# Kernel optimization log

Measured on AMD Instinct MI355X. Metric: run time of the kernel, lower is better.

Reference implementation:

```python
import jax, jax.numpy as jnp
import numpy as np

B, S, D, H, K, R = 16, 512, 768, 12, 16, 32
NS = 128  # LSH sample size = min(128, S//2)
HD = D // H

def _ln(t, g, b):
    m = t.mean(-1, keepdims=True)
    v = t.var(-1, keepdims=True)
    return (t - m) / jnp.sqrt(v + 1e-5) * g + b

def setup_inputs() -> dict:
    key = jax.random.key(0)
    ks = jax.random.split(key, 16)
    n = lambda k, shp: jax.random.normal(k, shp, jnp.float32) * 0.02
    return {
        'x': jax.random.normal(ks[0], (B, S, D), jnp.float32),
        'sample_idx': jax.random.randint(ks[1], (NS,), 0, S, jnp.int32),
        'w1': n(ks[2], (6, D // 4)), 'b1': jnp.zeros(D // 4, jnp.float32),
        'w2': n(ks[3], (D // 4, R)), 'b2': jnp.zeros(R, jnp.float32),
        'wd0': n(ks[4], (R, R)), 'bd0': jnp.zeros(R, jnp.float32),
        'wd1': n(ks[5], (R, R)), 'bd1': jnp.zeros(R, jnp.float32),
        'in_proj_w': n(ks[6], (D, 3 * D)), 'in_proj_b': jnp.zeros(3 * D, jnp.float32),
        'out_proj_w': n(ks[7], (D, D)), 'out_proj_b': jnp.zeros(D, jnp.float32),
        'topo_w': n(ks[8], (R, D)), 'topo_b': jnp.zeros(D, jnp.float32),
        'topo_gate': jnp.float32(0.1),
        'ln1_g': jnp.ones(D, jnp.float32), 'ln1_b': jnp.zeros(D, jnp.float32),
        'ln2_g': jnp.ones(D, jnp.float32), 'ln2_b': jnp.zeros(D, jnp.float32),
        'ffn_w1': n(ks[9], (D, 2 * D)), 'ffn_b1': jnp.zeros(2 * D, jnp.float32),
        'ffn_w2': n(ks[10], (2 * D, D)), 'ffn_b2': jnp.zeros(D, jnp.float32),
    }

def reference(x, sample_idx, w1, b1, w2, b2, wd0, bd0, wd1, bd1,
              in_proj_w, in_proj_b, out_proj_w, out_proj_b,
              topo_w, topo_b, topo_gate, ln1_g, ln1_b, ln2_g, ln2_b,
              ffn_w1, ffn_b1, ffn_w2, ffn_b2):
    # --- FastLSH._lsh_knn (S > 256 path): cdist to 128 sampled tokens + topk smallest ---
    s = jnp.take(x, sample_idx, axis=1)                                   # [B,NS,D]
    d2 = (jnp.sum(x * x, -1)[:, :, None] + jnp.sum(s * s, -1)[:, None, :]
          - 2.0 * jnp.einsum('bnd,bmd->bnm', x, s))                       # [B,S,NS]
    dist = jnp.sqrt(jnp.maximum(d2, 0.0))
    neg_top, _nbr = jax.lax.top_k(-dist, K)
    knn_dist = -neg_top                                                   # [B,S,K]
    # --- SimplifiedPersistenceComputer: scalar stats per batch (torch uses .item(), detached) ---
    df = knn_dist.reshape(B, -1)
    mean = df.mean(1); std = df.std(1, ddof=1)                            # torch.std is unbiased
    mn = df.min(1); mx = df.max(1)
    stats0 = jax.lax.stop_gradient(
        jnp.stack([mean, std, mn, mx, mean / 2, std / 2], -1))            # [B,6]
    # --- FastPersistenceLandscape: only dim-0 landscape feeds attention ---
    land0 = (jax.nn.relu(stats0 @ w1 + b1) @ w2 + b2) @ wd0 + bd0         # [B,R]
    # --- TopologicalAttention: MHA self-attention + gated topo embedding ---
    qkv = x @ in_proj_w + in_proj_b                                       # [B,S,3D]
    q, k, v = jnp.split(qkv, 3, axis=-1)
    hsplit = lambda t: t.reshape(B, S, H, HD).transpose(0, 2, 1, 3)
    q, k, v = hsplit(q), hsplit(k), hsplit(v)
    p = jax.nn.softmax(jnp.einsum('bhqd,bhkd->bhqk', q, k) / jnp.sqrt(jnp.float32(HD)), -1)
    o = jnp.einsum('bhqk,bhkd->bhqd', p, v).transpose(0, 2, 1, 3).reshape(B, S, D)
    attn = o @ out_proj_w + out_proj_b
    topo = land0 @ topo_w + topo_b                                        # [B,D]
    attn_out = attn + topo_gate * topo[:, None, :]
    # --- post-norm residual + FFN (GELU exact) ---
    x1 = _ln(x + attn_out, ln1_g, ln1_b)
    ffn = jax.nn.gelu(x1 @ ffn_w1 + ffn_b1, approximate=False) @ ffn_w2 + ffn_b2
    return _ln(x1 + ffn, ln2_g, ln2_b)
```

## Files before the change

### kernel.cpp

```cpp
#include <hip/hip_runtime.h>
#include <math.h>

#define Bz 16
#define Sz 512
#define Dz 768
#define Hz 12
#define HDz 64
#define Kz 16
#define NSz 128
#define Rz 32

typedef __attribute__((ext_vector_type(4))) float f32x4;
typedef __attribute__((ext_vector_type(8))) short bf16x8;

__device__ __forceinline__ unsigned short f2bf(float f) {
    unsigned u = __float_as_uint(f);
    return (unsigned short)((u + 0x7fffu + ((u >> 16) & 1u)) >> 16);
}
__device__ __forceinline__ float bf2f(unsigned short s) {
    return __uint_as_float(((unsigned)s) << 16);
}
__device__ __forceinline__ unsigned pk2(float a, float b) {
    return (unsigned)f2bf(a) | ((unsigned)f2bf(b) << 16);
}
__device__ __forceinline__ void gload_lds16(const void* g, void* l) {
    __builtin_amdgcn_global_load_lds(
        (const __attribute__((address_space(1))) unsigned int*)g,
        (__attribute__((address_space(3))) unsigned int*)l, 16, 0, 0);
}

__global__ __launch_bounds__(256) void xrn_k(const float* __restrict__ x, short* __restrict__ xb,
                                             float* __restrict__ xsq) {
    int wv = threadIdx.x >> 6, lane = threadIdx.x & 63;
    int row = blockIdx.x * 4 + wv;
    const float* r = x + (size_t)row * Dz;
    unsigned long long* dst = (unsigned long long*)(xb + (size_t)row * Dz);
    float s = 0.f;
#pragma unroll
    for (int j = 0; j < 3; j++) {
        float4 v = ((const float4*)r)[lane + j * 64];
        s += v.x * v.x + v.y * v.y + v.z * v.z + v.w * v.w;
        dst[lane + j * 64] = (unsigned long long)pk2(v.x, v.y) | ((unsigned long long)pk2(v.z, v.w) << 32);
    }
#pragma unroll
    for (int off = 32; off > 0; off >>= 1) s += __shfl_xor(s, off, 64);
    if (lane == 0) xsq[row] = s;
}

__device__ __forceinline__ void wtrans_body(const float* __restrict__ src, short* __restrict__ dst,
                                            int K, int N, int k0, int n0, int tid,
                                            float (*t)[65]) {
#pragma unroll
    for (int i = 0; i < 16; i++) {
        int e = tid + 256 * i;
        int kk = e >> 6, nn = e & 63;
        t[kk][nn] = src[(size_t)(k0 + kk) * N + n0 + nn];
    }
    __syncthreads();
#pragma unroll
    for (int i = 0; i < 16; i++) {
        int e = tid + 256 * i;
        int nn = e >> 6, kk = e & 63;
        dst[(size_t)(n0 + nn) * K + k0 + kk] = (short)f2bf(t[kk][nn]);
    }
}

__global__ __launch_bounds__(256) void prep_k(const float* __restrict__ ipw, const float* __restrict__ opw,
                                              const float* __restrict__ f1w, const float* __restrict__ f2w,
                                              short* __restrict__ wT_ip, short* __restrict__ wT_op,
                                              short* __restrict__ wT_f1, short* __restrict__ wT_f2,
                                              const float* __restrict__ x, const int* __restrict__ sidx,
                                              short* __restrict__ scb) {
    __shared__ float t[64][65];
    int bid = blockIdx.x, tid = threadIdx.x;
    if (bid < 432) {
        int lo = bid, tx = lo % 36, ty = lo / 36;
        wtrans_body(ipw, wT_ip, Dz, 3 * Dz, ty * 64, tx * 64, tid, t);
    } else if (bid < 576) {
        int lo = bid - 432, tx = lo % 12, ty = lo / 12;
        wtrans_body(opw, wT_op, Dz, Dz, ty * 64, tx * 64, tid, t);
    } else if (bid < 864) {
        int lo = bid - 576, tx = lo % 24, ty = lo / 24;
        wtrans_body(f1w, wT_f1, Dz, 2 * Dz, ty * 64, tx * 64, tid, t);
    } else if (bid < 1152) {
        int lo = bid - 864, tx = lo % 12, ty = lo / 12;
        wtrans_body(f2w, wT_f2, 2 * Dz, Dz, ty * 64, tx * 64, tid, t);
    } else {
        int gb = bid - 1152;
        int row = gb * 16 + (tid >> 4);
        int b = row >> 7, jj = row & 127;
        const float* src = x + ((size_t)(b * Sz) + sidx[jj]) * Dz;
        unsigned long long* dr = (unsigned long long*)(scb + (size_t)row * Dz);
        int l16 = tid & 15;
#pragma unroll
        for (int j = 0; j < 12; j++) {
            int idx = j * 16 + l16;
            float4 v = ((const float4*)src)[idx];
            dr[idx] = (unsigned long long)pk2(v.x, v.y) | ((unsigned long long)pk2(v.z, v.w) << 32);
        }
    }
}

__global__ __launch_bounds__(128) void knnstat_k(const float* __restrict__ D, float4* __restrict__ rowred) {
    __shared__ float dv[NSz];
    __shared__ float red[NSz], red2[NSz];
    __shared__ float rmin, rmax;
    int tid = threadIdx.x, row = blockIdx.x;
    float dist = D[(size_t)row * NSz + tid];
    dv[tid] = dist;
    __syncthreads();
    int rank = 0;
#pragma unroll 8
    for (int j = 0; j < NSz; j++) {
        float o = dv[j];
        rank += (o < dist) || (o == dist && j < tid);
    }
    if (rank == 0) rmin = dist;
    if (rank == Kz - 1) rmax = dist;
    red[tid] = (rank < Kz) ? dist : 0.f;
    red2[tid] = (rank < Kz) ? dist * dist : 0.f;
    __syncthreads();
    for (int st = 64; st > 0; st >>= 1) {
        if (tid < st) { red[tid] += red[tid + st]; red2[tid] += red2[tid + st]; }
        __syncthreads();
    }
    if (tid == 0) rowred[row] = make_float4(red[0], red2[0], rmin, rmax);
}

__global__ __launch_bounds__(256) void land_topo_k(const float4* __restrict__ rowred,
                                                   const float* __restrict__ w1, const float* __restrict__ b1,
                                                   const float* __restrict__ w2, const float* __restrict__ b2,
                                                   const float* __restrict__ wd0, const float* __restrict__ bd0,
                                                   const float* __restrict__ topo_w, const float* __restrict__ topo_b,
                                                   const float* gate, float* __restrict__ topo_add) {
    __shared__ float4 red4[256];
    __shared__ float st[6];
    __shared__ float h[Dz / 4];
    __shared__ float l2[Rz];
    __shared__ float land[Rz];
    int b = blockIdx.x, tid = threadIdx.x;
    float4 a = rowred[b * Sz + tid];
    float4 c = rowred[b * Sz + 256 + tid];
    float4 r;
    r.x = a.x + c.x; r.y = a.y + c.y;
    r.z = fminf(a.z, c.z); r.w = fmaxf(a.w, c.w);
    red4[tid] = r;
    __syncthreads();
    for (int stp = 128; stp > 0; stp >>= 1) {
        if (tid < stp) {
            float4 p = red4[tid], q = red4[tid + stp];
            p.x += q.x; p.y += q.y; p.z = fminf(p.z, q.z); p.w = fmaxf(p.w, q.w);
            red4[tid] = p;
        }
        __syncthreads();
    }
    if (tid == 0) {
        const double N = (double)(Sz * Kz);
        double sum = (double)red4[0].x, sumsq = (double)red4[0].y;
        double mean = sum / N;
        double var = (sumsq - N * mean * mean) / (N - 1.0);
        float sd = (float)sqrt(fmax(var, 0.0));
        float m = (float)mean;
        st[0] = m; st[1] = sd;
        st[2] = red4[0].z; st[3] = red4[0].w;
        st[4] = m * 0.5f; st[5] = sd * 0.5f;
    }
    __syncthreads();
    if (tid < Dz / 4) {
        float a1 = b1[tid];
#pragma unroll
        for (int i = 0; i < 6; i++) a1 += st[i] * w1[i * (Dz / 4) + tid];
        h[tid] = fmaxf(a1, 0.f);
    }
    __syncthreads();
    if (tid < Rz) {
        float a1 = b2[tid];
        for (int i = 0; i < Dz / 4; i++) a1 += h[i] * w2[i * Rz + tid];
        l2[tid] = a1;
    }
    __syncthreads();
    if (tid < Rz) {
        float a1 = bd0[tid];
#pragma unroll
        for (int i = 0; i < Rz; i++) a1 += l2[i] * wd0[i * Rz + tid];
        land[tid] = a1;
    }
    __syncthreads();
    float g = gate[0];
    for (int d = tid; d < Dz; d += 256) {
        float a1 = topo_b[d];
#pragma unroll
        for (int i = 0; i < Rz; i++) a1 += land[i] * topo_w[i * Dz + d];
        topo_add[b * Dz + d] = g * a1;
    }
}

__device__ __forceinline__ void stage_tile(const short* gbase, int ldk, int row0, int k0,
                                           short* ldsbase, int w, int l) {
#pragma unroll
    for (int c = 0; c < 2; c++) {
        int r = c * 64 + w * 16 + (l >> 2);
        int qg = (l & 3) ^ ((r >> 1) & 3);
        const short* src = gbase + (size_t)(row0 + r) * ldk + k0 + qg * 8;
        gload_lds16(src, ldsbase + (c * 4 + w) * 512);
    }
}

template <int EPI>
__global__ __launch_bounds__(256) void mgemm_k(const short* __restrict__ A, const short* __restrict__ BT,
                                               const float* __restrict__ bias,
                                               float* __restrict__ C, short* __restrict__ Cb,
                                               int N, int Kd, int gx,
                                               short* __restrict__ qo, short* __restrict__ ko,
                                               short* __restrict__ vT,
                                               const int* __restrict__ sidx, const float* __restrict__ xsq) {
    __shared__ short lds[2][2][4096];
    int tid = threadIdx.x, w = tid >> 6, l = tid & 63;
    int nwg = gridDim.x, q = nwg >> 3;
    int orig = (blockIdx.x & 7) * q + (blockIdx.x >> 3);
    int m0 = (orig / gx) * 128, n0 = (orig % gx) * 128;
    const short* BTb = BT;
    if (EPI == 4) BTb += (size_t)(m0 >> 9) * NSz * Kd;
    int wr = w >> 1, wc = w & 1, g = l >> 4, ql = l & 15;
    f32x4 acc[4][4];
#pragma unroll
    for (int i = 0; i < 4; i++)
#pragma unroll
        for (int j = 0; j < 4; j++) acc[i][j] = (f32x4){0.f, 0.f, 0.f, 0.f};
    stage_tile(A, Kd, m0, 0, lds[0][0], w, l);
    stage_tile(BTb, Kd, n0, 0, lds[0][1], w, l);
    __syncthreads();
    int nst = Kd / 32;
    for (int t = 0; t < nst; t++) {
        int buf = t & 1;
        if (t + 1 < nst) {
            stage_tile(A, Kd, m0, (t + 1) * 32, lds[buf ^ 1][0], w, l);
            stage_tile(BTb, Kd, n0, (t + 1) * 32, lds[buf ^ 1][1], w, l);
        }
        bf16x8 af[4], bfr[4];
#pragma unroll
        for (int i = 0; i < 4; i++) {
            int r = wr * 64 + i * 16 + ql;
            af[i] = *(const bf16x8*)((const char*)lds[buf][0] + r * 64 + ((g ^ ((r >> 1) & 3)) << 4));
        }
#pragma unroll
        for (int j = 0; j < 4; j++) {
            int r = wc * 64 + j * 16 + ql;
            bfr[j] = *(const bf16x8*)((const char*)lds[buf][1] + r * 64 + ((g ^ ((r >> 1) & 3)) << 4));
        }
#pragma unroll
        for (int i = 0; i < 4; i++)
#pragma unroll
            for (int j = 0; j < 4; j++)
                acc[i][j] = __builtin_amdgcn_mfma_f32_16x16x32_bf16(af[i], bfr[j], acc[i][j], 0, 0, 0);
        __syncthreads();
    }

    if (EPI == 4) {
#pragma unroll
        for (int i = 0; i < 4; i++) {
            int rowb = m0 + wr * 64 + i * 16 + g * 4;
#pragma unroll
            for (int j = 0; j < 4; j++) {
                int col = wc * 64 + j * 16 + ql;
                float ssq = xsq[((rowb >> 9) << 9) + sidx[col]];
#pragma unroll
                for (int r = 0; r < 4; r++) {
                    int row = rowb + r;
                    float d2 = xsq[row] + ssq - 2.f * acc[i][j][r];
                    C[(size_t)row * NSz + col] = sqrtf(fmaxf(d2, 0.f));
                }
            }
        }
    } else {
        short* cl = (short*)lds;
        const int part = (EPI == 2) ? (n0 / Dz) : 0;
        const bool cm = (EPI == 2) && (part == 2);
        if (!cm) {
#pragma unroll
            for (int i = 0; i < 4; i++) {
#pragma unroll
                for (int j = 0; j < 4; j++) {
                    int colL = wc * 64 + j * 16 + ql;
                    float bsv = bias[n0 + colL];
#pragma unroll
                    for (int r = 0; r < 4; r++) {
                        int rowL = wr * 64 + i * 16 + g * 4 + r;
                        float val = acc[i][j][r] + bsv;
                        if (EPI == 1) val = 0.5f * val * (1.f + erff(val * 0.70710678118654752f));
                        cl[rowL * 128 + (((colL >> 3) ^ (rowL & 15)) << 3) + (colL & 7)] = (short)f2bf(val);
                    }
                }
            }
        } else {
#pragma unroll
            for (int i = 0; i < 4; i++) {
#pragma unroll
                for (int j = 0; j < 4; j++) {
                    int colL = wc * 64 + j * 16 + ql;
                    float bsv = bias[n0 + colL];
                    int row4 = wr * 64 + i * 16 + g * 4;
                    unsigned long long u =
                        (unsigned long long)pk2(acc[i][j][0] + bsv, acc[i][j][1] + bsv)
                      | ((unsigned long long)pk2(acc[i][j][2] + bsv, acc[i][j][3] + bsv) << 32);
                    *(unsigned long long*)((char*)cl +
                        colL * 256 + (((row4 >> 3) ^ (colL & 15)) << 4) + (row4 & 7) * 2) = u;
                }
            }
        }
        __syncthreads();
#pragma unroll
        for (int it = 0; it < 8; it++) {
            int c = tid + 256 * it;
            int a = c >> 4, sl = c & 15;
            bf16x8 vv = *(const bf16x8*)(cl + a * 128 + ((sl ^ (a & 15)) << 3));
            if (EPI == 1 || EPI == 3) {
                *(bf16x8*)(Cb + (size_t)(m0 + a) * N + n0 + sl * 8) = vv;
            } else if (!cm) {
                int rr = m0 + a;
                int b = rr >> 9, s = rr & 511;
                int h = ((n0 % Dz) >> 6) + (sl >> 3);
                short* dst = part ? ko : qo;
                *(bf16x8*)(dst + (((size_t)(b * Hz + h)) * Sz + s) * HDz + (sl & 7) * 8) = vv;
            } else {
                int wi = (n0 - 2 * Dz) + a;
                int h = wi >> 6, hd = wi & 63;
                int b = m0 >> 9, s0 = (m0 & 511) + sl * 8;
                *(bf16x8*)(vT + ((size_t)(b * Hz + h) * HDz + hd) * Sz + s0) = vv;
            }
        }
    }
}

__global__ __launch_bounds__(256, 4) void attn4_k(const short* __restrict__ Q, const short* __restrict__ Kt,
                                                  const short* __restrict__ Vt, short* __restrict__ O) {
    __shared__ short kl[2][4096];
    __shared__ short vl[2][4096];
    __shared__ char plds[4][2048];
    int tid = threadIdx.x, w = tid >> 6, l = tid & 63;
    int bh = blockIdx.x % (Bz * Hz), qt = blockIdx.x / (Bz * Hz);
    int g = l >> 4, ql = l & 15;
    const short* qb = Q + (size_t)bh * (Sz * HDz) + (size_t)(qt * 64 + w * 16) * HDz;
    const short* kb = Kt + (size_t)bh * (Sz * HDz);
    const short* vb = Vt + (size_t)bh * (HDz * Sz);
    bf16x8 qf0 = *(const bf16x8*)(qb + (size_t)ql * HDz + g * 8);
    bf16x8 qf1 = *(const bf16x8*)(qb + (size_t)ql * HDz + 32 + g * 8);
    f32x4 oa[4];
#pragma unroll
    for (int m = 0; m < 4; m++) oa[m] = (f32x4){0.f, 0.f, 0.f, 0.f};
    float psum = 0.f;

    auto stage = [&](int c, int bb) {
#pragma unroll
        for (int it = 0; it < 2; it++) {
            int i = (it * 4 + w) * 64 + l;
            int row = i >> 3;
            int ss = (i & 7) ^ (row & 7);
            gload_lds16(kb + (size_t)(c * 64 + row) * HDz + ss * 8,
                        (char*)kl[bb] + (it * 4 + w) * 1024);
            gload_lds16(vb + (size_t)row * Sz + c * 64 + ss * 8,
                        (char*)vl[bb] + (it * 4 + w) * 1024);
        }
    };

    stage(0, 0);
    __syncthreads();
    char* pw = plds[w];
#pragma unroll
    for (int c = 0; c < 8; c++) {
        int cur = c & 1;
        if (c < 7) stage(c + 1, cur ^ 1);
        const char* kc = (const char*)kl[cur];
        const char* vc = (const char*)vl[cur];
#pragma unroll
        for (int tl = 0; tl < 4; tl++) {
            int row = tl * 16 + ql;
            bf16x8 a0 = *(const bf16x8*)(kc + row * 128 + ((g ^ (ql & 7)) << 4));
            bf16x8 a1 = *(const bf16x8*)(kc + row * 128 + (((4 + g) ^ (ql & 7)) << 4));
            f32x4 s4 = (f32x4){0.f, 0.f, 0.f, 0.f};
            s4 = __builtin_amdgcn_mfma_f32_16x16x32_bf16(a0, qf0, s4, 0, 0, 0);
            s4 = __builtin_amdgcn_mfma_f32_16x16x32_bf16(a1, qf1, s4, 0, 0, 0);
            float e0 = __expf(s4[0] * 0.125f);
            float e1 = __expf(s4[1] * 0.125f);
            float e2 = __expf(s4[2] * 0.125f);
            float e3 = __expf(s4[3] * 0.125f);
            psum += (e0 + e1) + (e2 + e3);
            int slot = (tl * 2 + (g >> 1)) ^ (ql & 7);
            *(unsigned long long*)(pw + ql * 128 + slot * 16 + (g & 1) * 8)
                = (unsigned long long)pk2(e0, e1) | ((unsigned long long)pk2(e2, e3) << 32);
        }
#pragma unroll
        for (int s = 0; s < 2; s++) {
            int slot = (s * 4 + g) ^ (ql & 7);
            bf16x8 pb = *(const bf16x8*)(pw + ql * 128 + slot * 16);
#pragma unroll
            for (int m = 0; m < 4; m++) {
                int row = m * 16 + ql;
                bf16x8 va = *(const bf16x8*)(vc + row * 128 + (((s * 4 + g) ^ (ql & 7)) << 4));
                oa[m] = __builtin_amdgcn_mfma_f32_16x16x32_bf16(va, pb, oa[m], 0, 0, 0);
            }
        }
        __syncthreads();
    }
    psum += __shfl_xor(psum, 16, 64);
    psum += __shfl_xor(psum, 32, 64);
    float inv = 1.f / psum;
    int b = bh / Hz, h = bh % Hz;
    int s = qt * 64 + w * 16 + ql;
#pragma unroll
    for (int m = 0; m < 4; m++)
#pragma unroll
        for (int j = 0; j < 2; j++) {
            float v0 = oa[m][j * 2] * inv, v1 = oa[m][j * 2 + 1] * inv;
            unsigned u = pk2(v0, v1);
            int d = h * 64 + m * 16 + g * 4 + j * 2;
            *(unsigned*)((char*)O + 2 * ((size_t)(b * Sz + s) * Dz + d)) = u;
        }
}

__global__ __launch_bounds__(256) void ln1_k(const float* __restrict__ x, const short* __restrict__ ap,
                                             const float* __restrict__ topo,
                                             const float* __restrict__ gam, const float* __restrict__ bet,
                                             short* __restrict__ x1b) {
    __shared__ float buf[Dz];
    __shared__ float red[256];
    int row = blockIdx.x, tid = threadIdx.x, b = row >> 9;
    float s = 0.f;
    for (int i = tid; i < Dz; i += 256) {
        float vv = x[(size_t)row * Dz + i] + bf2f((unsigned short)ap[(size_t)row * Dz + i]) + topo[b * Dz + i];
        buf[i] = vv; s += vv;
    }
    red[tid] = s; __syncthreads();
    for (int st = 128; st > 0; st >>= 1) { if (tid < st) red[tid] += red[tid + st]; __syncthreads(); }
    float mean = red[0] / (float)Dz;
    __syncthreads();
    float s2 = 0.f;
    for (int i = tid; i < Dz; i += 256) { float d = buf[i] - mean; s2 += d * d; }
    red[tid] = s2; __syncthreads();
    for (int st = 128; st > 0; st >>= 1) { if (tid < st) red[tid] += red[tid + st]; __syncthreads(); }
    float inv = 1.f / sqrtf(red[0] / (float)Dz + 1e-5f);
    for (int i = tid; i < Dz; i += 256)
        x1b[(size_t)row * Dz + i] = (short)f2bf((buf[i] - mean) * inv * gam[i] + bet[i]);
}

__global__ __launch_bounds__(256) void ln2_k(const short* __restrict__ x1b, const short* __restrict__ f2,
                                             const float* __restrict__ gam, const float* __restrict__ bet,
                                             float* __restrict__ out) {
    __shared__ float buf[Dz];
    __shared__ float red[256];
    int row = blockIdx.x, tid = threadIdx.x;
    float s = 0.f;
    for (int i = tid; i < Dz; i += 256) {
        float vv = bf2f((unsigned short)x1b[(size_t)row * Dz + i]) + bf2f((unsigned short)f2[(size_t)row * Dz + i]);
        buf[i] = vv; s += vv;
    }
    red[tid] = s; __syncthreads();
    for (int st = 128; st > 0; st >>= 1) { if (tid < st) red[tid] += red[tid + st]; __syncthreads(); }
    float mean = red[0] / (float)Dz;
    __syncthreads();
    float s2 = 0.f;
    for (int i = tid; i < Dz; i += 256) { float d = buf[i] - mean; s2 += d * d; }
    red[tid] = s2; __syncthreads();
    for (int st = 128; st > 0; st >>= 1) { if (tid < st) red[tid] += red[tid + st]; __syncthreads(); }
    float inv = 1.f / sqrtf(red[0] / (float)Dz + 1e-5f);
    for (int i = tid; i < Dz; i += 256)
        out[(size_t)row * Dz + i] = (buf[i] - mean) * inv * gam[i] + bet[i];
}

extern "C" void kernel_launch(void* const* d_in, const int* in_sizes, int n_in,
                              void* d_out, int out_size, void* d_ws, size_t ws_size,
                              hipStream_t stream) {
    const float* x          = (const float*)d_in[0];
    const int*   sidx       = (const int*)d_in[1];
    const float* w1         = (const float*)d_in[2];
    const float* b1         = (const float*)d_in[3];
    const float* w2         = (const float*)d_in[4];
    const float* b2         = (const float*)d_in[5];
    const float* wd0        = (const float*)d_in[6];
    const float* bd0        = (const float*)d_in[7];
    const float* in_proj_w  = (const float*)d_in[10];
    const float* in_proj_b  = (const float*)d_in[11];
    const float* out_proj_w = (const float*)d_in[12];
    const float* out_proj_b = (const float*)d_in[13];
    const float* topo_w     = (const float*)d_in[14];
    const float* topo_b     = (const float*)d_in[15];
    const float* gate       = (const float*)d_in[16];
    const float* ln1_g      = (const float*)d_in[17];
    const float* ln1_b      = (const float*)d_in[18];
    const float* ln2_g      = (const float*)d_in[19];
    const float* ln2_b      = (const float*)d_in[20];
    const float* ffn_w1     = (const float*)d_in[21];
    const float* ffn_b1     = (const float*)d_in[22];
    const float* ffn_w2     = (const float*)d_in[23];
    const float* ffn_b2     = (const float*)d_in[24];

    char* w = (char*)d_ws;
    float4* rowred = (float4*)(w + 0);
    float*  xsq    = (float*)(w + 131072);
    float*  topo_add = (float*)(w + 163840);
    size_t off = 212992;
    short* wT_ip = (short*)(w + off); off += (size_t)3 * Dz * Dz * 2;
    short* wT_op = (short*)(w + off); off += (size_t)Dz * Dz * 2;
    short* wT_f1 = (short*)(w + off); off += (size_t)2 * Dz * Dz * 2;
    short* wT_f2 = (short*)(w + off); off += (size_t)2 * Dz * Dz * 2;
    short* scb   = (short*)(w + off); off += (size_t)Bz * NSz * Dz * 2;
    float* Dd    = (float*)(w + off); off += (size_t)Bz * Sz * NSz * 4;
    char*  qkv0  = w + off;           off += (size_t)3 * Bz * Sz * Dz * 2;
    short* qbuf  = (short*)qkv0;
    short* kbuf  = (short*)(qkv0 + (size_t)Bz * Sz * Dz * 2);
    short* vTbuf = (short*)(qkv0 + (size_t)2 * Bz * Sz * Dz * 2);
    short* x1b   = (short*)qkv0;
    short* hb    = (short*)(qkv0 + (size_t)Bz * Sz * Dz * 2);
    short* xb    = (short*)(w + off); off += (size_t)Bz * Sz * Dz * 2;
    short* ob    = xb;
    short* apb   = (short*)(w + off); off += (size_t)Bz * Sz * Dz * 2;
    short* f2b   = (short*)(w + off); off += (size_t)Bz * Sz * Dz * 2;

    const int M = Bz * Sz;

    xrn_k<<<M / 4, 256, 0, stream>>>(x, xb, xsq);
    prep_k<<<1280, 256, 0, stream>>>(in_proj_w, out_proj_w, ffn_w1, ffn_w2,
                                     wT_ip, wT_op, wT_f1, wT_f2, x, sidx, scb);
    mgemm_k<4><<<M / 128, 256, 0, stream>>>(xb, scb, nullptr, Dd, nullptr,
                                            NSz, Dz, 1, nullptr, nullptr, nullptr, sidx, xsq);
    knnstat_k<<<M, 128, 0, stream>>>(Dd, rowred);
    land_topo_k<<<Bz, 256, 0, stream>>>(rowred, w1, b1, w2, b2,
                                        wd0, bd0, topo_w, topo_b, gate, topo_add);
    mgemm_k<2><<<(3 * Dz / 128) * (M / 128), 256, 0, stream>>>(xb, wT_ip, in_proj_b,
                                                               nullptr, nullptr, 3 * Dz, Dz, 3 * Dz / 128,
                                                               qbuf, kbuf, vTbuf, nullptr, nullptr);
    attn4_k<<<Bz * Hz * 8, 256, 0, stream>>>(qbuf, kbuf, vTbuf, ob);
    mgemm_k<3><<<(Dz / 128) * (M / 128), 256, 0, stream>>>(ob, wT_op, out_proj_b,
                                                           nullptr, apb, Dz, Dz, Dz / 128,
                                                           nullptr, nullptr, nullptr, nullptr, nullptr);
    ln1_k<<<M, 256, 0, stream>>>(x, apb, topo_add, ln1_g, ln1_b, x1b);
    mgemm_k<1><<<(2 * Dz / 128) * (M / 128), 256, 0, stream>>>(x1b, wT_f1, ffn_b1,
                                                               nullptr, hb, 2 * Dz, Dz, 2 * Dz / 128,
                                                               nullptr, nullptr, nullptr, nullptr, nullptr);
    mgemm_k<3><<<(Dz / 128) * (M / 128), 256, 0, stream>>>(hb, wT_f2, ffn_b2,
                                                           nullptr, f2b, Dz, 2 * Dz, Dz / 128,
                                                           nullptr, nullptr, nullptr, nullptr, nullptr);
    ln2_k<<<M, 256, 0, stream>>>(x1b, f2b, ln2_g, ln2_b, (float*)d_out);
}
```

Baseline: 399.1 us.

## Use 256x128 GEMM tiles with 512 threads and warp-per-row layernorms

The GEMM kernel now uses 512-thread blocks covering 256x128 output tiles, with one combined staging routine loading both operand tiles. The epilogue is done in two halves through the shared buffer. This doubles reuse of the B tile per block and halves the grid size. Separately, both layernorm kernels are rewritten so each wavefront handles one row with vectorized loads, a single-pass sum and sum-of-squares, and shuffle reductions instead of shared-memory tree reductions. The single-pass variance changes numerics slightly, and the smaller GEMM grids may underfill the GPU.

```diff
diff --git a/kernel.cpp b/kernel.cpp
--- a/kernel.cpp
+++ b/kernel.cpp
@@ -195,30 +195,37 @@
     }
 }
 
-__device__ __forceinline__ void stage_tile(const short* gbase, int ldk, int row0, int k0,
-                                           short* ldsbase, int w, int l) {
-#pragma unroll
-    for (int c = 0; c < 2; c++) {
-        int r = c * 64 + w * 16 + (l >> 2);
-        int qg = (l & 3) ^ ((r >> 1) & 3);
-        const short* src = gbase + (size_t)(row0 + r) * ldk + k0 + qg * 8;
-        gload_lds16(src, ldsbase + (c * 4 + w) * 512);
+__device__ __forceinline__ void stage_tile256(const short* __restrict__ A, const short* __restrict__ B,
+                                              int ldk, int m0, int n0, int k0,
+                                              short* lbase, int w, int l) {
+#pragma unroll
+    for (int si = 0; si < 3; si++) {
+        int s = si * 8 + w;
+        if (s < 16) {
+            int r = s * 16 + (l >> 2);
+            int qg = (l & 3) ^ ((r >> 1) & 3);
+            gload_lds16(A + (size_t)(m0 + r) * ldk + k0 + qg * 8, lbase + s * 512);
+        } else {
+            int r = (s - 16) * 16 + (l >> 2);
+            int qg = (l & 3) ^ ((r >> 1) & 3);
+            gload_lds16(B + (size_t)(n0 + r) * ldk + k0 + qg * 8, lbase + 8192 + (s - 16) * 512);
+        }
     }
 }
 
 template <int EPI>
-__global__ __launch_bounds__(256) void mgemm_k(const short* __restrict__ A, const short* __restrict__ BT,
+__global__ __launch_bounds__(512) void mgemm_k(const short* __restrict__ A, const short* __restrict__ BT,
                                                const float* __restrict__ bias,
                                                float* __restrict__ C, short* __restrict__ Cb,
                                                int N, int Kd, int gx,
                                                short* __restrict__ qo, short* __restrict__ ko,
                                                short* __restrict__ vT,
                                                const int* __restrict__ sidx, const float* __restrict__ xsq) {
-    __shared__ short lds[2][2][4096];
+    __shared__ short lds[2][12288];
     int tid = threadIdx.x, w = tid >> 6, l = tid & 63;
     int nwg = gridDim.x, q = nwg >> 3;
     int orig = (blockIdx.x & 7) * q + (blockIdx.x >> 3);
-    int m0 = (orig / gx) * 128, n0 = (orig % gx) * 128;
+    int m0 = (orig / gx) * 256, n0 = (orig % gx) * 128;
     const short* BTb = BT;
     if (EPI == 4) BTb += (size_t)(m0 >> 9) * NSz * Kd;
     int wr = w >> 1, wc = w & 1, g = l >> 4, ql = l & 15;
@@ -227,26 +234,23 @@
     for (int i = 0; i < 4; i++)
 #pragma unroll
         for (int j = 0; j < 4; j++) acc[i][j] = (f32x4){0.f, 0.f, 0.f, 0.f};
-    stage_tile(A, Kd, m0, 0, lds[0][0], w, l);
-    stage_tile(BTb, Kd, n0, 0, lds[0][1], w, l);
+    stage_tile256(A, BTb, Kd, m0, n0, 0, lds[0], w, l);
     __syncthreads();
     int nst = Kd / 32;
     for (int t = 0; t < nst; t++) {
         int buf = t & 1;
-        if (t + 1 < nst) {
-            stage_tile(A, Kd, m0, (t + 1) * 32, lds[buf ^ 1][0], w, l);
-            stage_tile(BTb, Kd, n0, (t + 1) * 32, lds[buf ^ 1][1], w, l);
-        }
+        if (t + 1 < nst)
+            stage_tile256(A, BTb, Kd, m0, n0, (t + 1) * 32, lds[buf ^ 1], w, l);
         bf16x8 af[4], bfr[4];
 #pragma unroll
         for (int i = 0; i < 4; i++) {
             int r = wr * 64 + i * 16 + ql;
-            af[i] = *(const bf16x8*)((const char*)lds[buf][0] + r * 64 + ((g ^ ((r >> 1) & 3)) << 4));
+            af[i] = *(const bf16x8*)((const char*)lds[buf] + r * 64 + ((g ^ ((r >> 1) & 3)) << 4));
         }
 #pragma unroll
         for (int j = 0; j < 4; j++) {
             int r = wc * 64 + j * 16 + ql;
-            bfr[j] = *(const bf16x8*)((const char*)lds[buf][1] + r * 64 + ((g ^ ((r >> 1) & 3)) << 4));
+            bfr[j] = *(const bf16x8*)((const char*)lds[buf] + 16384 + r * 64 + ((g ^ ((r >> 1) & 3)) << 4));
         }
 #pragma unroll
         for (int i = 0; i < 4; i++)
@@ -260,10 +264,11 @@
 #pragma unroll
         for (int i = 0; i < 4; i++) {
             int rowb = m0 + wr * 64 + i * 16 + g * 4;
+            int bb = rowb >> 9;
 #pragma unroll
             for (int j = 0; j < 4; j++) {
                 int col = wc * 64 + j * 16 + ql;
-                float ssq = xsq[((rowb >> 9) << 9) + sidx[col]];
+                float ssq = xsq[(bb << 9) + sidx[col]];
 #pragma unroll
                 for (int r = 0; r < 4; r++) {
                     int row = rowb + r;
@@ -273,61 +278,69 @@
             }
         }
     } else {
-        short* cl = (short*)lds;
+        short* cl = lds[0];
         const int part = (EPI == 2) ? (n0 / Dz) : 0;
         const bool cm = (EPI == 2) && (part == 2);
-        if (!cm) {
-#pragma unroll
-            for (int i = 0; i < 4; i++) {
-#pragma unroll
-                for (int j = 0; j < 4; j++) {
-                    int colL = wc * 64 + j * 16 + ql;
-                    float bsv = bias[n0 + colL];
-#pragma unroll
-                    for (int r = 0; r < 4; r++) {
-                        int rowL = wr * 64 + i * 16 + g * 4 + r;
-                        float val = acc[i][j][r] + bsv;
-                        if (EPI == 1) val = 0.5f * val * (1.f + erff(val * 0.70710678118654752f));
-                        cl[rowL * 128 + (((colL >> 3) ^ (rowL & 15)) << 3) + (colL & 7)] = (short)f2bf(val);
+#pragma unroll
+        for (int h = 0; h < 2; h++) {
+            if ((w >> 2) == h) {
+                int wrl = wr & 1;
+                if (!cm) {
+#pragma unroll
+                    for (int i = 0; i < 4; i++) {
+#pragma unroll
+                        for (int j = 0; j < 4; j++) {
+                            int colL = wc * 64 + j * 16 + ql;
+                            float bsv = bias[n0 + colL];
+#pragma unroll
+                            for (int r = 0; r < 4; r++) {
+                                int rowL = wrl * 64 + i * 16 + g * 4 + r;
+                                float val = acc[i][j][r] + bsv;
+                                if (EPI == 1) val = 0.5f * val * (1.f + erff(val * 0.70710678118654752f));
+                                cl[rowL * 128 + (((colL >> 3) ^ (rowL & 15)) << 3) + (colL & 7)] = (short)f2bf(val);
+                            }
+                        }
+                    }
+                } else {
+#pragma unroll
+                    for (int i = 0; i < 4; i++) {
+#pragma unroll
+                        for (int j = 0; j < 4; j++) {
+                            int colL = wc * 64 + j * 16 + ql;
+                            float bsv = bias[n0 + colL];
+                            int row4 = wrl * 64 + i * 16 + g * 4;
+                            unsigned long long u =
+                                (unsigned long long)pk2(acc[i][j][0] + bsv, acc[i][j][1] + bsv)
+                              | ((unsigned long long)pk2(acc[i][j][2] + bsv, acc[i][j][3] + bsv) << 32);
+                            *(unsigned long long*)((char*)cl +
+                                colL * 256 + (((row4 >> 3) ^ (colL & 15)) << 4) + (row4 & 7) * 2) = u;
+                        }
                     }
                 }
             }
-        } else {
-#pragma unroll
-            for (int i = 0; i < 4; i++) {
-#pragma unroll
-                for (int j = 0; j < 4; j++) {
-                    int colL = wc * 64 + j * 16 + ql;
-                    float bsv = bias[n0 + colL];
-                    int row4 = wr * 64 + i * 16 + g * 4;
-                    unsigned long long u =
-                        (unsigned long long)pk2(acc[i][j][0] + bsv, acc[i][j][1] + bsv)
-                      | ((unsigned long long)pk2(acc[i][j][2] + bsv, acc[i][j][3] + bsv) << 32);
-                    *(unsigned long long*)((char*)cl +
-                        colL * 256 + (((row4 >> 3) ^ (colL & 15)) << 4) + (row4 & 7) * 2) = u;
+            __syncthreads();
+            int rbase = m0 + h * 128;
+#pragma unroll
+            for (int it = 0; it < 4; it++) {
+                int c = tid + 512 * it;
+                int a = c >> 4, sl = c & 15;
+                bf16x8 vv = *(const bf16x8*)(cl + a * 128 + ((sl ^ (a & 15)) << 3));
+                if (EPI == 1 || EPI == 3) {
+                    *(bf16x8*)(Cb + (size_t)(rbase + a) * N + n0 + sl * 8) = vv;
+                } else if (!cm) {
+                    int rr = rbase + a;
+                    int b = rr >> 9, s = rr & 511;
+                    int hh = ((n0 % Dz) >> 6) + (sl >> 3);
+                    short* dst = part ? ko : qo;
+                    *(bf16x8*)(dst + (((size_t)(b * Hz + hh)) * Sz + s) * HDz + (sl & 7) * 8) = vv;
+                } else {
+                    int wi = (n0 - 2 * Dz) + a;
+                    int hh = wi >> 6, hd = wi & 63;
+                    int b = rbase >> 9, s0 = (rbase & 511) + sl * 8;
+                    *(bf16x8*)(vT + ((size_t)(b * Hz + hh) * HDz + hd) * Sz + s0) = vv;
                 }
             }
-        }
-        __syncthreads();
-#pragma unroll
-        for (int it = 0; it < 8; it++) {
-            int c = tid + 256 * it;
-            int a = c >> 4, sl = c & 15;
-            bf16x8 vv = *(const bf16x8*)(cl + a * 128 + ((sl ^ (a & 15)) << 3));
-            if (EPI == 1 || EPI == 3) {
-                *(bf16x8*)(Cb + (size_t)(m0 + a) * N + n0 + sl * 8) = vv;
-            } else if (!cm) {
-                int rr = m0 + a;
-                int b = rr >> 9, s = rr & 511;
-                int h = ((n0 % Dz) >> 6) + (sl >> 3);
-                short* dst = part ? ko : qo;
-                *(bf16x8*)(dst + (((size_t)(b * Hz + h)) * Sz + s) * HDz + (sl & 7) * 8) = vv;
-            } else {
-                int wi = (n0 - 2 * Dz) + a;
-                int h = wi >> 6, hd = wi & 63;
-                int b = m0 >> 9, s0 = (m0 & 511) + sl * 8;
-                *(bf16x8*)(vT + ((size_t)(b * Hz + h) * HDz + hd) * Sz + s0) = vv;
-            }
+            if (h == 0) __syncthreads();
         }
     }
 }
@@ -422,49 +435,92 @@
                                              const float* __restrict__ topo,
                                              const float* __restrict__ gam, const float* __restrict__ bet,
                                              short* __restrict__ x1b) {
-    __shared__ float buf[Dz];
-    __shared__ float red[256];
-    int row = blockIdx.x, tid = threadIdx.x, b = row >> 9;
-    float s = 0.f;
-    for (int i = tid; i < Dz; i += 256) {
-        float vv = x[(size_t)row * Dz + i] + bf2f((unsigned short)ap[(size_t)row * Dz + i]) + topo[b * Dz + i];
-        buf[i] = vv; s += vv;
-    }
-    red[tid] = s; __syncthreads();
-    for (int st = 128; st > 0; st >>= 1) { if (tid < st) red[tid] += red[tid + st]; __syncthreads(); }
-    float mean = red[0] / (float)Dz;
-    __syncthreads();
-    float s2 = 0.f;
-    for (int i = tid; i < Dz; i += 256) { float d = buf[i] - mean; s2 += d * d; }
-    red[tid] = s2; __syncthreads();
-    for (int st = 128; st > 0; st >>= 1) { if (tid < st) red[tid] += red[tid + st]; __syncthreads(); }
-    float inv = 1.f / sqrtf(red[0] / (float)Dz + 1e-5f);
-    for (int i = tid; i < Dz; i += 256)
-        x1b[(size_t)row * Dz + i] = (short)f2bf((buf[i] - mean) * inv * gam[i] + bet[i]);
+    int wv = threadIdx.x >> 6, lane = threadIdx.x & 63;
+    int row = blockIdx.x * 4 + wv, b = row >> 9;
+    const float4* xr = (const float4*)(x + (size_t)row * Dz);
+    const float4* tr = (const float4*)(topo + (size_t)b * Dz);
+    const unsigned long long* ar = (const unsigned long long*)(ap + (size_t)row * Dz);
+    float v[12];
+    float sum = 0.f, ssq = 0.f;
+#pragma unroll
+    for (int j = 0; j < 3; j++) {
+        int idx = lane + j * 64;
+        float4 xv = xr[idx];
+        float4 tv = tr[idx];
+        unsigned long long av = ar[idx];
+        float v0 = xv.x + bf2f((unsigned short)av) + tv.x;
+        float v1 = xv.y + bf2f((unsigned short)(av >> 16)) + tv.y;
+        float v2 = xv.z + bf2f((unsigned short)(av >> 32)) + tv.z;
+        float v3 = xv.w + bf2f((unsigned short)(av >> 48)) + tv.w;
+        v[j * 4 + 0] = v0; v[j * 4 + 1] = v1; v[j * 4 + 2] = v2; v[j * 4 + 3] = v3;
+        sum += (v0 + v1) + (v2 + v3);
+        ssq += (v0 * v0 + v1 * v1) + (v2 * v2 + v3 * v3);
+    }
+#pragma unroll
+    for (int off = 32; off > 0; off >>= 1) {
+        sum += __shfl_xor(sum, off, 64);
+        ssq += __shfl_xor(ssq, off, 64);
+    }
+    float mean = sum * (1.f / (float)Dz);
+    float var = ssq * (1.f / (float)Dz) - mean * mean;
+    float inv = 1.f / sqrtf(var + 1e-5f);
+    unsigned long long* dst = (unsigned long long*)(x1b + (size_t)row * Dz);
+#pragma unroll
+    for (int j = 0; j < 3; j++) {
+        int idx = lane + j * 64;
+        float4 gv = ((const float4*)gam)[idx];
+        float4 bv = ((const float4*)bet)[idx];
+        float o0 = (v[j * 4 + 0] - mean) * inv * gv.x + bv.x;
+        float o1 = (v[j * 4 + 1] - mean) * inv * gv.y + bv.y;
+        float o2 = (v[j * 4 + 2] - mean) * inv * gv.z + bv.z;
+        float o3 = (v[j * 4 + 3] - mean) * inv * gv.w + bv.w;
+        dst[idx] = (unsigned long long)pk2(o0, o1) | ((unsigned long long)pk2(o2, o3) << 32);
+    }
 }
 
 __global__ __launch_bounds__(256) void ln2_k(const short* __restrict__ x1b, const short* __restrict__ f2,
                                              const float* __restrict__ gam, const float* __restrict__ bet,
                                              float* __restrict__ out) {
-    __shared__ float buf[Dz];
-    __shared__ float red[256];
-    int row = blockIdx.x, tid = threadIdx.x;
-    float s = 0.f;
-    for (int i = tid; i < Dz; i += 256) {
-        float vv = bf2f((unsigned short)x1b[(size_t)row * Dz + i]) + bf2f((unsigned short)f2[(size_t)row * Dz + i]);
-        buf[i] = vv; s += vv;
-    }
-    red[tid] = s; __syncthreads();
-    for (int st = 128; st > 0; st >>= 1) { if (tid < st) red[tid] += red[tid + st]; __syncthreads(); }
-    float mean = red[0] / (float)Dz;
-    __syncthreads();
-    float s2 = 0.f;
-    for (int i = tid; i < Dz; i += 256) { float d = buf[i] - mean; s2 += d * d; }
-    red[tid] = s2; __syncthreads();
-    for (int st = 128; st > 0; st >>= 1) { if (tid < st) red[tid] += red[tid + st]; __syncthreads(); }
-    float inv = 1.f / sqrtf(red[0] / (float)Dz + 1e-5f);
-    for (int i = tid; i < Dz; i += 256)
-        out[(size_t)row * Dz + i] = (buf[i] - mean) * inv * gam[i] + bet[i];
+    int wv = threadIdx.x >> 6, lane = threadIdx.x & 63;
+    int row = blockIdx.x * 4 + wv;
+    const unsigned long long* xr = (const unsigned long long*)(x1b + (size_t)row * Dz);
+    const unsigned long long* fr = (const unsigned long long*)(f2 + (size_t)row * Dz);
+    float v[12];
+    float sum = 0.f, ssq = 0.f;
+#pragma unroll
+    for (int j = 0; j < 3; j++) {
+        int idx = lane + j * 64;
+        unsigned long long xv = xr[idx];
+        unsigned long long fv = fr[idx];
+        float v0 = bf2f((unsigned short)xv) + bf2f((unsigned short)fv);
+        float v1 = bf2f((unsigned short)(xv >> 16)) + bf2f((unsigned short)(fv >> 16));
+        float v2 = bf2f((unsigned short)(xv >> 32)) + bf2f((unsigned short)(fv >> 32));
+        float v3 = bf2f((unsigned short)(xv >> 48)) + bf2f((unsigned short)(fv >> 48));
+        v[j * 4 + 0] = v0; v[j * 4 + 1] = v1; v[j * 4 + 2] = v2; v[j * 4 + 3] = v3;
+        sum += (v0 + v1) + (v2 + v3);
+        ssq += (v0 * v0 + v1 * v1) + (v2 * v2 + v3 * v3);
+    }
+#pragma unroll
+    for (int off = 32; off > 0; off >>= 1) {
+        sum += __shfl_xor(sum, off, 64);
+        ssq += __shfl_xor(ssq, off, 64);
+    }
+    float mean = sum * (1.f / (float)Dz);
+    float var = ssq * (1.f / (float)Dz) - mean * mean;
+    float inv = 1.f / sqrtf(var + 1e-5f);
+    float4* dst = (float4*)(out + (size_t)row * Dz);
+#pragma unroll
+    for (int j = 0; j < 3; j++) {
+        int idx = lane + j * 64;
+        float4 gv = ((const float4*)gam)[idx];
+        float4 bv = ((const float4*)bet)[idx];
+        float4 o;
+        o.x = (v[j * 4 + 0] - mean) * inv * gv.x + bv.x;
+        o.y = (v[j * 4 + 1] - mean) * inv * gv.y + bv.y;
+        o.z = (v[j * 4 + 2] - mean) * inv * gv.z + bv.z;
+        o.w = (v[j * 4 + 3] - mean) * inv * gv.w + bv.w;
+        dst[idx] = o;
+    }
 }
 
 extern "C" void kernel_launch(void* const* d_in, const int* in_sizes, int n_in,
@@ -521,24 +577,24 @@
     xrn_k<<<M / 4, 256, 0, stream>>>(x, xb, xsq);
     prep_k<<<1280, 256, 0, stream>>>(in_proj_w, out_proj_w, ffn_w1, ffn_w2,
                                      wT_ip, wT_op, wT_f1, wT_f2, x, sidx, scb);
-    mgemm_k<4><<<M / 128, 256, 0, stream>>>(xb, scb, nullptr, Dd, nullptr,
+    mgemm_k<4><<<M / 256, 512, 0, stream>>>(xb, scb, nullptr, Dd, nullptr,
                                             NSz, Dz, 1, nullptr, nullptr, nullptr, sidx, xsq);
     knnstat_k<<<M, 128, 0, stream>>>(Dd, rowred);
     land_topo_k<<<Bz, 256, 0, stream>>>(rowred, w1, b1, w2, b2,
                                         wd0, bd0, topo_w, topo_b, gate, topo_add);
-    mgemm_k<2><<<(3 * Dz / 128) * (M / 128), 256, 0, stream>>>(xb, wT_ip, in_proj_b,
+    mgemm_k<2><<<(3 * Dz / 128) * (M / 256), 512, 0, stream>>>(xb, wT_ip, in_proj_b,
                                                                nullptr, nullptr, 3 * Dz, Dz, 3 * Dz / 128,
                                                                qbuf, kbuf, vTbuf, nullptr, nullptr);
     attn4_k<<<Bz * Hz * 8, 256, 0, stream>>>(qbuf, kbuf, vTbuf, ob);
-    mgemm_k<3><<<(Dz / 128) * (M / 128), 256, 0, stream>>>(ob, wT_op, out_proj_b,
+    mgemm_k<3><<<(Dz / 128) * (M / 256), 512, 0, stream>>>(ob, wT_op, out_proj_b,
                                                            nullptr, apb, Dz, Dz, Dz / 128,
                                                            nullptr, nullptr, nullptr, nullptr, nullptr);
-    ln1_k<<<M, 256, 0, stream>>>(x, apb, topo_add, ln1_g, ln1_b, x1b);
-    mgemm_k<1><<<(2 * Dz / 128) * (M / 128), 256, 0, stream>>>(x1b, wT_f1, ffn_b1,
+    ln1_k<<<M / 4, 256, 0, stream>>>(x, apb, topo_add, ln1_g, ln1_b, x1b);
+    mgemm_k<1><<<(2 * Dz / 128) * (M / 256), 512, 0, stream>>>(x1b, wT_f1, ffn_b1,
                                                                nullptr, hb, 2 * Dz, Dz, 2 * Dz / 128,
                                                                nullptr, nullptr, nullptr, nullptr, nullptr);
-    mgemm_k<3><<<(Dz / 128) * (M / 128), 256, 0, stream>>>(hb, wT_f2, ffn_b2,
+    mgemm_k<3><<<(Dz / 128) * (M / 256), 512, 0, stream>>>(hb, wT_f2, ffn_b2,
                                                            nullptr, f2b, Dz, 2 * Dz, Dz / 128,
                                                            nullptr, nullptr, nullptr, nullptr, nullptr);
-    ln2_k<<<M, 256, 0, stream>>>(x1b, f2b, ln2_g, ln2_b, (float*)d_out);
-}
+    ln2_k<<<M / 4, 256, 0, stream>>>(x1b, f2b, ln2_g, ln2_b, (float*)d_out);
+}
```

After: 400.5 us. About the same (+0.3%).
